# Optimization experiments

Hardware: AMD Instinct MI355X
Metric: run time of the kernel (lower is better)

The kernel has to match this reference:

```python
import jax, jax.numpy as jnp
import numpy as np

N = 50000      # nodes
E = 400000     # edges
DIM = 3        # pseudo-coordinate dim
M = 3          # kernel size per dim (closed B-spline, degree 1)
K = M ** DIM   # 27 basis weights
IN = 32
MID = 32
OUT = 32
EPS = 1e-5


def spline_basis(edge_attr):
    """Degree-1 closed B-spline basis. edge_attr: [E, DIM] in [0,1].
    Returns basis [E, 2^DIM], weight indices [E, 2^DIM] into K."""
    bits = (jnp.arange(2 ** DIM)[:, None] >> jnp.arange(DIM)[None, :]) & 1  # [8, DIM]
    scaled = edge_attr * M                       # closed spline: scale by kernel size
    lo = jnp.floor(scaled)
    frac = scaled - lo                           # [E, DIM]
    b = jnp.where(bits[None].astype(bool), frac[:, None, :], 1.0 - frac[:, None, :])
    basis = jnp.prod(b, axis=-1)                 # [E, 8]
    idx = (lo.astype(jnp.int32)[:, None, :] + bits[None]) % M  # [E, 8, DIM]
    strides = M ** jnp.arange(DIM)               # [1, 3, 9]
    widx = jnp.sum(idx * strides, axis=-1)       # [E, 8] in [0, K)
    return basis, widx


def spline_conv(x, src, dst, basis, widx, W, root, bias):
    """x: [N, in]; W: [K, in, out]; mean aggregation + root weight + bias."""
    x_j = x[src]                                          # gather [E, in]
    upd = basis[:, :, None] * x_j[:, None, :]             # [E, 8, in]
    # scatter-add basis-weighted source features into per-(node, weight-idx) bins
    S = jnp.zeros((N, K, x.shape[1]), x.dtype).at[dst[:, None], widx].add(upd)
    deg = jnp.zeros((N,), x.dtype).at[dst].add(1.0)
    deg = jnp.maximum(deg, 1.0)
    msg = jnp.einsum('nki,kio->no', S, W) / deg[:, None]  # mean over incoming edges
    return msg + x @ root + bias


def batchnorm(h, gamma, beta):
    mu = jnp.mean(h, axis=0)
    var = jnp.var(h, axis=0)  # biased, as in torch BN forward
    return (h - mu) * jax.lax.rsqrt(var + EPS) * gamma + beta


def setup_inputs() -> dict:
    key = jax.random.key(0)
    ks = jax.random.split(key, 16)
    d = {}
    d['x'] = jax.random.normal(ks[0], (N, IN), jnp.float32)
    d['edge_index'] = jax.random.randint(ks[1], (2, E), 0, N, dtype=jnp.int32)
    d['edge_attr'] = jax.random.uniform(ks[2], (E, DIM), dtype=jnp.float32)
    d['pos'] = jax.random.normal(ks[3], (N, DIM), jnp.float32)
    def wscale(fan_in):
        return 1.0 / np.sqrt(fan_in)
    d['W1'] = jax.random.normal(ks[4], (K, IN, MID), jnp.float32) * wscale(IN)
    d['root1'] = jax.random.normal(ks[5], (IN, MID), jnp.float32) * wscale(IN)
    d['b1'] = jnp.zeros((MID,), jnp.float32)
    d['W2'] = jax.random.normal(ks[6], (K, MID, 2 * MID), jnp.float32) * wscale(MID)
    d['root2'] = jax.random.normal(ks[7], (MID, 2 * MID), jnp.float32) * wscale(MID)
    d['b2'] = jnp.zeros((2 * MID,), jnp.float32)
    d['gamma'] = jnp.ones((2 * MID,), jnp.float32)
    d['beta'] = jnp.zeros((2 * MID,), jnp.float32)
    c3_in = 2 * MID + 3
    d['W3'] = jax.random.normal(ks[8], (K, c3_in, OUT), jnp.float32) * wscale(c3_in)
    d['root3'] = jax.random.normal(ks[9], (c3_in, OUT), jnp.float32) * wscale(c3_in)
    d['b3'] = jnp.zeros((OUT,), jnp.float32)
    return d


def reference(x, edge_index, edge_attr, pos, W1, root1, b1, W2, root2, b2,
              gamma, beta, W3, root3, b3):
    src, dst = edge_index[0], edge_index[1]
    basis, widx = spline_basis(edge_attr)
    h = jax.nn.elu(spline_conv(x, src, dst, basis, widx, W1, root1, b1))
    h = jax.nn.elu(batchnorm(spline_conv(h, src, dst, basis, widx, W2, root2, b2), gamma, beta))
    h = jnp.concatenate([h, pos], axis=1)
    out = spline_conv(h, src, dst, basis, widx, W3, root3, b3)
    return out
```

## Files before the change

### kernel.cpp

```cpp
#include <hip/hip_runtime.h>
#include <hip/hip_bf16.h>


#define EPS 1e-5f
#define MAXN 50176
#define MAXE 401408
#define SP2 904
#define SP3 2696

typedef __attribute__((ext_vector_type(8))) short short8;
typedef __attribute__((ext_vector_type(4))) float floatx4;

__device__ int             g_deg[MAXN];
__device__ int             g_offs[MAXN + 1];
__device__ int             g_cursor[MAXN];
__device__ int             g_bsum[256];
__device__ int             g_esrc[MAXE];
__device__ __align__(16) uint4 g_ebas[MAXE * 4];
__device__ __align__(16) __hip_bfloat16 g_h0[MAXN * 32];
__device__ __align__(16) __hip_bfloat16 g_h1[MAXN * 32];
__device__ __align__(16) __hip_bfloat16 g_h2[MAXN * 64];
__device__ __align__(16) __hip_bfloat16 g_h3[MAXN * 96];
__device__ __align__(16) __hip_bfloat16 g_Wp1[28672];
__device__ __align__(16) __hip_bfloat16 g_Wp2[57344];
__device__ __align__(16) __hip_bfloat16 g_Wp3[86016];
__device__ float           g_stats[128];
__device__ int             g_isbf16;

__device__ __forceinline__ float loadf(const void* p, int i, bool bf)
{
    return bf ? (float)((const __hip_bfloat16*)p)[i] : ((const float*)p)[i];
}
__device__ __forceinline__ float bf16f(unsigned int u)
{
    return __uint_as_float(u << 16);
}
__device__ __forceinline__ unsigned short bfbits(float f)
{
    union { __hip_bfloat16 h; unsigned short u; } cv;
    cv.h = __float2bfloat16(f);
    return cv.u;
}

__global__ void init_detect(const unsigned int* __restrict__ x, int n)
{
    int i = blockIdx.x * blockDim.x + threadIdx.x;
    if (blockIdx.x == 0 && threadIdx.x < 64) {
        int lane = threadIdx.x;
        int cnt = 0;
        for (int k = lane; k < 256; k += 64) {
            unsigned int lo = x[k] & 0xFFFFu;
            int ex = (int)((lo >> 7) & 0xFFu);
            if (lo == 0u || (ex >= 96 && ex <= 140)) cnt++;
        }
#pragma unroll
        for (int o = 1; o < 64; o <<= 1) cnt += __shfl_xor(cnt, o, 64);
        if (lane == 0) g_isbf16 = (cnt >= 200) ? 1 : 0;
    }
    if (i < n) { g_deg[i] = 0; g_cursor[i] = 0; }
    if (i < 128) g_stats[i] = 0.0f;
}

template <int COUT>
__device__ __forceinline__ void prep_ws_dev(const void* W, const void* root,
                                            __hip_bfloat16* Wp, int t, bool bf)
{
    int j = t & 7;
    int lane = (t >> 3) & 63;
    int rest = t >> 9;
    int kk = rest % 28;
    int nt = rest / 28;
    int k = kk * 32 + (lane >> 4) * 8 + j;
    int o = nt * 16 + (lane & 15);
    float v;
    if (k < 864) {
        int bin = k >> 5, p = k & 31;
        int ch = 2 * (p & 15) + (p >> 4);
        v = loadf(W, (bin * 32 + ch) * COUT + o, bf);
    } else {
        int p = k - 864;
        int ch = 2 * (p & 15) + (p >> 4);
        v = loadf(root, ch * COUT + o, bf);
    }
    Wp[t] = __float2bfloat16(v);
}

__device__ __forceinline__ void prep_w3_dev(const void* W, const void* root,
                                            __hip_bfloat16* Wp, int t, bool bf)
{
    const int KB = 84;
    int j = t & 7;
    int lane = (t >> 3) & 63;
    int rest = t >> 9;
    int kk = rest % KB;
    int nt = rest / KB;
    int k = kk * 32 + (lane >> 4) * 8 + j;
    int o = nt * 16 + (lane & 15);
    float v = 0.0f;
    if (k < 2592) {
        int bin = k / 96;
        int p = k - bin * 96;
        int ch = 6 * (p & 15) + (p >> 4);
        if (ch < 67) v = loadf(W, (bin * 67 + ch) * 32 + o, bf);
    } else {
        int p = k - 2592;
        int ch = 6 * (p & 15) + (p >> 4);
        if (ch < 67) v = loadf(root, ch * 32 + o, bf);
    }
    Wp[t] = __float2bfloat16(v);
}

__global__ void misc_kernel(const int* __restrict__ dst, const void* __restrict__ x,
                            const void* W1, const void* r1,
                            const void* W2, const void* r2,
                            const void* W3, const void* r3, int E, int N)
{
    int t = blockIdx.x * blockDim.x + threadIdx.x;
    const bool bf = (g_isbf16 != 0);
    if (t < E) { atomicAdd(&g_deg[dst[t]], 1); return; }
    t -= E;
    int nx = N * 32;
    if (t < nx) { g_h0[t] = __float2bfloat16(loadf(x, t, bf)); return; }
    t -= nx;
    if (t < 28672) { prep_ws_dev<32>(W1, r1, g_Wp1, t, bf); return; }
    t -= 28672;
    if (t < 57344) { prep_ws_dev<64>(W2, r2, g_Wp2, t, bf); return; }
    t -= 57344;
    if (t < 86016) { prep_w3_dev(W3, r3, g_Wp3, t, bf); return; }
}

__global__ void scan_blk(int n)
{
    __shared__ int buf[256];
    int tid = threadIdx.x;
    int i = blockIdx.x * 256 + tid;
    int v = (i < n) ? g_deg[i] : 0;
    buf[tid] = v;
    __syncthreads();
    for (int o = 1; o < 256; o <<= 1) {
        int t = (tid >= o) ? buf[tid - o] : 0;
        __syncthreads();
        buf[tid] += t;
        __syncthreads();
    }
    if (i < n) g_offs[i] = buf[tid] - v;
    if (tid == 255) g_bsum[blockIdx.x] = buf[255];
}

__global__ void scan_top(int nb, int n)
{
    __shared__ int buf[256];
    int tid = threadIdx.x;
    int v = (tid < nb) ? g_bsum[tid] : 0;
    buf[tid] = v;
    __syncthreads();
    for (int o = 1; o < 256; o <<= 1) {
        int t = (tid >= o) ? buf[tid - o] : 0;
        __syncthreads();
        buf[tid] += t;
        __syncthreads();
    }
    if (tid < nb) g_bsum[tid] = buf[tid] - v;
    if (tid == nb - 1) g_offs[n] = buf[tid];
}

__global__ void scan_add(int n)
{
    int i = blockIdx.x * 256 + threadIdx.x;
    if (i < n) g_offs[i] += g_bsum[i >> 8];
}

__global__ void basis_fill(const void* __restrict__ attr,
                           const int* __restrict__ src,
                           const int* __restrict__ dst, int E)
{
    int e = blockIdx.x * blockDim.x + threadIdx.x;
    if (e >= E) return;
    const bool bf = (g_isbf16 != 0);
    float f[3];
    int lo[3];
#pragma unroll
    for (int d = 0; d < 3; ++d) {
        float a = loadf(attr, e * 3 + d, bf);
        float s = a * 3.0f;
        float l = floorf(s);
        lo[d] = (int)l;
        f[d] = s - l;
    }
    const int p3[3] = {1, 3, 9};
    int wx8[8];
    unsigned short bb[8];
#pragma unroll
    for (int b = 0; b < 8; ++b) {
        float w = 1.0f;
        int id = 0;
#pragma unroll
        for (int d = 0; d < 3; ++d) {
            int bit = (b >> d) & 1;
            w *= bit ? f[d] : (1.0f - f[d]);
            id += ((lo[d] + bit) % 3) * p3[d];
        }
        wx8[b] = id;
        bb[b] = bfbits(w);
    }
    unsigned wds[16];
#pragma unroll
    for (int i = 0; i < 16; ++i) {
        unsigned w = 0;
#pragma unroll
        for (int b = 0; b < 8; ++b) {
            if (wx8[b] == i)      w |= (unsigned)bb[b];
            if (wx8[b] == i + 16) w |= (unsigned)bb[b] << 16;
        }
        wds[i] = w;
    }
    int d = dst[e];
    int p = atomicAdd(&g_cursor[d], 1);
    int slot = g_offs[d] + p;
    uint4* out4 = &g_ebas[(size_t)slot * 4];
    out4[0] = make_uint4(wds[0],  wds[1],  wds[2],  wds[3]);
    out4[1] = make_uint4(wds[4],  wds[5],  wds[6],  wds[7]);
    out4[2] = make_uint4(wds[8],  wds[9],  wds[10], wds[11]);
    out4[3] = make_uint4(wds[12], wds[13], wds[14], wds[15]);
    g_esrc[slot] = src[e];
}

template <int COUT, bool ELU, int IN_SEL, int OUT_SEL>
__global__ __launch_bounds__(512, 8) void fused_conv(const void* __restrict__ bias,
                                                     int N)
{
    __shared__ unsigned short Sb[8 * SP2];
    __shared__ __align__(16) unsigned basb[8][16][16];
    __shared__ int ssrc[8][16];
    __shared__ float invd[8];
    int tid = threadIdx.x, wid = tid >> 6, lane = tid & 63;
    int nbase = blockIdx.x * 8;
    const bool bf = (g_isbf16 != 0);
    const unsigned short* xptr = (IN_SEL == 0) ? (const unsigned short*)g_h0
                                               : (const unsigned short*)g_h1;
    const __hip_bfloat16* Wp = (COUT == 32) ? g_Wp1 : g_Wp2;

    int n = nbase + wid;
    int m = lane & 15, quad = lane >> 4;

    if (n < N) {
        int e0 = g_offs[n], e1 = g_offs[n + 1];
        floatx4 C00 = {}, C01 = {}, C10 = {}, C11 = {};
        for (int base = e0; base < e1; base += 16) {
            int cnt = e1 - base; if (cnt > 16) cnt = 16;
            {
                int es = lane >> 2, part = lane & 3;
                uint4 v = make_uint4(0, 0, 0, 0);
                if (es < cnt) v = g_ebas[(size_t)(base + es) * 4 + part];
                *(uint4*)&basb[wid][es][part * 4] = v;
                if (lane < 16)
                    ssrc[wid][lane] = (lane < cnt) ? g_esrc[base + lane] : 0;
            }
            __builtin_amdgcn_s_waitcnt(0);
            int jmax = (cnt + 3) >> 2;
            unsigned a0w[4] = {0, 0, 0, 0}, a1w[4] = {0, 0, 0, 0};
            unsigned b0w[4] = {0, 0, 0, 0}, b1w[4] = {0, 0, 0, 0};
#pragma unroll
            for (int j = 0; j < 4; ++j) {
                if (j >= jmax) break;
                int kidx = j * 4 + quad;
                int sn = ssrc[wid][kidx];
                unsigned pw = basb[wid][kidx][m];
                unsigned hw = *((const unsigned*)xptr + (size_t)sn * 16 + m);
                unsigned sh = 16 * (j & 1);
                a0w[j >> 1] |= (hw & 0xFFFFu) << sh;
                a1w[j >> 1] |= (hw >> 16) << sh;
                b0w[j >> 1] |= (pw & 0xFFFFu) << sh;
                b1w[j >> 1] |= (pw >> 16) << sh;
            }
            union U { unsigned w[4]; short8 v; } A0, A1, B0, B1;
#pragma unroll
            for (int q = 0; q < 4; ++q) {
                A0.w[q] = a0w[q]; A1.w[q] = a1w[q];
                B0.w[q] = b0w[q]; B1.w[q] = b1w[q];
            }
            C00 = __builtin_amdgcn_mfma_f32_16x16x32_bf16(A0.v, B0.v, C00, 0, 0, 0);
            C01 = __builtin_amdgcn_mfma_f32_16x16x32_bf16(A0.v, B1.v, C01, 0, 0, 0);
            C10 = __builtin_amdgcn_mfma_f32_16x16x32_bf16(A1.v, B0.v, C10, 0, 0, 0);
            C11 = __builtin_amdgcn_mfma_f32_16x16x32_bf16(A1.v, B1.v, C11, 0, 0, 0);
        }
        unsigned short* Srow = Sb + wid * SP2;
        {
            floatx4 Cf[4] = {C00, C01, C10, C11};
#pragma unroll
            for (int f = 0; f < 4; ++f) {
                int mt = f >> 1, nt = f & 1;
                int bin = nt * 16 + m;
                if (bin < 27) {
                    union { unsigned short h[4]; uint2 u; } pk;
#pragma unroll
                    for (int r = 0; r < 4; ++r) pk.h[r] = bfbits(Cf[f][r]);
                    *(uint2*)(Srow + bin * 32 + mt * 16 + quad * 4) = pk.u;
                }
            }
        }
        if (lane < 32) {
            int ch = 2 * (lane & 15) + (lane >> 4);
            Srow[864 + lane] = xptr[(size_t)n * 32 + ch];
        }
        if (lane == 0) {
            int deg = e1 - e0;
            invd[wid] = 1.0f / (float)(deg < 1 ? 1 : deg);
        }
    }
    __syncthreads();

    if (wid * 16 < COUT) {
        int mrow = m & 7;
        const unsigned short* Ab = Sb + mrow * SP2 + quad * 8;
        floatx4 accS = {}, accR = {};
#pragma unroll
        for (int kk = 0; kk < 28; ++kk) {
            short8 a = *(const short8*)(Ab + kk * 32);
            const short* bp = (const short*)Wp +
                ((size_t)(wid * 28 + kk) * 64 + lane) * 8;
            short8 b = *(const short8*)bp;
            if (kk < 27) accS = __builtin_amdgcn_mfma_f32_16x16x32_bf16(a, b, accS, 0, 0, 0);
            else         accR = __builtin_amdgcn_mfma_f32_16x16x32_bf16(a, b, accR, 0, 0, 0);
        }
        int o = wid * 16 + m;
        float bval = loadf(bias, o, bf);
#pragma unroll
        for (int r = 0; r < 4; ++r) {
            int slot = quad * 4 + r;
            if (slot >= 8) continue;
            int nn = nbase + slot;
            if (nn >= N) continue;
            float v = accS[r] * invd[slot] + accR[r] + bval;
            if (ELU) v = v > 0.0f ? v : expm1f(v);
            if (OUT_SEL == 1) g_h1[nn * 32 + o] = __float2bfloat16(v);
            else              g_h2[nn * 64 + o] = __float2bfloat16(v);
        }
    }
}

__global__ __launch_bounds__(512, 4) void fused_conv3(const void* __restrict__ bias,
                                                      void* __restrict__ out_ext,
                                                      int N)
{
    __shared__ __align__(16) unsigned short Sb[8 * SP3];
    __shared__ __align__(16) union {
        struct { unsigned bas[8][16][16]; int src[8][16]; } s1;
        float red[6][64][4];
    } u;
    __shared__ float invd[8];
    int tid = threadIdx.x, wid = tid >> 6, lane = tid & 63;
    int nbase = blockIdx.x * 8;
    const bool bf = (g_isbf16 != 0);
    const unsigned short* xptr = (const unsigned short*)g_h3;

    int n = nbase + wid;
    int m = lane & 15, quad = lane >> 4;

    if (n < N) {
        int e0 = g_offs[n], e1 = g_offs[n + 1];
        floatx4 C[6][2];
#pragma unroll
        for (int t = 0; t < 6; ++t) {
            C[t][0] = (floatx4){0.f, 0.f, 0.f, 0.f};
            C[t][1] = (floatx4){0.f, 0.f, 0.f, 0.f};
        }
        for (int base = e0; base < e1; base += 16) {
            int cnt = e1 - base; if (cnt > 16) cnt = 16;
            {
                int es = lane >> 2, part = lane & 3;
                uint4 v = make_uint4(0, 0, 0, 0);
                if (es < cnt) v = g_ebas[(size_t)(base + es) * 4 + part];
                *(uint4*)&u.s1.bas[wid][es][part * 4] = v;
                if (lane < 16)
                    u.s1.src[wid][lane] = (lane < cnt) ? g_esrc[base + lane] : 0;
            }
            __builtin_amdgcn_s_waitcnt(0);
            int jmax = (cnt + 3) >> 2;
            unsigned aw[6][4] = {{0, 0, 0, 0}, {0, 0, 0, 0}, {0, 0, 0, 0},
                                 {0, 0, 0, 0}, {0, 0, 0, 0}, {0, 0, 0, 0}};
            unsigned b0w[4] = {0, 0, 0, 0}, b1w[4] = {0, 0, 0, 0};
#pragma unroll
            for (int j = 0; j < 4; ++j) {
                if (j >= jmax) break;
                int kidx = j * 4 + quad;
                int sn = u.s1.src[wid][kidx];
                unsigned pw = u.s1.bas[wid][kidx][m];
                const unsigned* hp = (const unsigned*)xptr + (size_t)sn * 48 + m * 3;
                unsigned h0 = hp[0], h1 = hp[1], h2 = hp[2];
                unsigned sh = 16 * (j & 1);
                int r = j >> 1;
                aw[0][r] |= (h0 & 0xFFFFu) << sh;
                aw[1][r] |= (h0 >> 16) << sh;
                aw[2][r] |= (h1 & 0xFFFFu) << sh;
                aw[3][r] |= (h1 >> 16) << sh;
                aw[4][r] |= (h2 & 0xFFFFu) << sh;
                aw[5][r] |= (h2 >> 16) << sh;
                b0w[r] |= (pw & 0xFFFFu) << sh;
                b1w[r] |= (pw >> 16) << sh;
            }
            union U { unsigned w[4]; short8 v; } A, B0, B1;
#pragma unroll
            for (int q = 0; q < 4; ++q) { B0.w[q] = b0w[q]; B1.w[q] = b1w[q]; }
#pragma unroll
            for (int t = 0; t < 6; ++t) {
#pragma unroll
                for (int q = 0; q < 4; ++q) A.w[q] = aw[t][q];
                C[t][0] = __builtin_amdgcn_mfma_f32_16x16x32_bf16(A.v, B0.v, C[t][0], 0, 0, 0);
                C[t][1] = __builtin_amdgcn_mfma_f32_16x16x32_bf16(A.v, B1.v, C[t][1], 0, 0, 0);
            }
        }
        unsigned short* Srow = Sb + wid * SP3;
#pragma unroll
        for (int t = 0; t < 6; ++t) {
#pragma unroll
            for (int ntile = 0; ntile < 2; ++ntile) {
                int bin = ntile * 16 + m;
                if (bin < 27) {
                    union { unsigned short h[4]; uint2 uu; } pk;
#pragma unroll
                    for (int r = 0; r < 4; ++r) pk.h[r] = bfbits(C[t][ntile][r]);
                    *(uint2*)(Srow + bin * 96 + t * 16 + quad * 4) = pk.uu;
                }
            }
        }
        for (int p = lane; p < 96; p += 64) {
            int ch = 6 * (p & 15) + (p >> 4);
            Srow[2592 + p] = xptr[(size_t)n * 96 + ch];
        }
        if (lane == 0) {
            int deg = e1 - e0;
            invd[wid] = 1.0f / (float)(deg < 1 ? 1 : deg);
        }
    }
    __syncthreads();

    int nt = wid & 1, kq = wid >> 1;
    int mrow = m & 7;
    const unsigned short* Ab = Sb + mrow * SP3 + quad * 8;
    floatx4 accS = {}, accR = {};
    {
        int kbeg = kq * 21, kend = kbeg + 21;
        int ksplit = (kend < 81) ? kend : 81;
        for (int kk = kbeg; kk < ksplit; ++kk) {
            short8 a = *(const short8*)(Ab + kk * 32);
            const short* bp = (const short*)g_Wp3 +
                ((size_t)(nt * 84 + kk) * 64 + lane) * 8;
            short8 b = *(const short8*)bp;
            accS = __builtin_amdgcn_mfma_f32_16x16x32_bf16(a, b, accS, 0, 0, 0);
        }
        for (int kk = ksplit; kk < kend; ++kk) {
            short8 a = *(const short8*)(Ab + kk * 32);
            const short* bp = (const short*)g_Wp3 +
                ((size_t)(nt * 84 + kk) * 64 + lane) * 8;
            short8 b = *(const short8*)bp;
            accR = __builtin_amdgcn_mfma_f32_16x16x32_bf16(a, b, accR, 0, 0, 0);
        }
    }
    if (kq < 3)
        *(floatx4*)&u.red[wid][lane][0] = accS;
    __syncthreads();
    if (kq == 3) {
#pragma unroll
        for (int w = 0; w < 3; ++w)
            accS += *(const floatx4*)&u.red[2 * w + nt][lane][0];
        int o = nt * 16 + m;
        float bval = loadf(bias, o, bf);
#pragma unroll
        for (int r = 0; r < 4; ++r) {
            int slot = quad * 4 + r;
            if (slot >= 8) continue;
            int nn = nbase + slot;
            if (nn >= N) continue;
            float v = accS[r] * invd[slot] + accR[r] + bval;
            if (bf) ((__hip_bfloat16*)out_ext)[nn * 32 + o] = __float2bfloat16(v);
            else    ((float*)out_ext)[nn * 32 + o] = v;
        }
    }
}

__global__ void bn_reduce(int n)
{
    int tid = threadIdx.x;
    int c = tid & 63;
    int r = tid >> 6;
    float s = 0.0f, s2 = 0.0f;
    for (int i = blockIdx.x * 4 + r; i < n; i += gridDim.x * 4) {
        float v = (float)g_h2[i * 64 + c];
        s += v; s2 += v * v;
    }
    __shared__ float b1s[256], b2s[256];
    b1s[tid] = s; b2s[tid] = s2;
    __syncthreads();
    if (r == 0) {
        s  = b1s[c] + b1s[c + 64] + b1s[c + 128] + b1s[c + 192];
        s2 = b2s[c] + b2s[c + 64] + b2s[c + 128] + b2s[c + 192];
        atomicAdd(&g_stats[c], s);
        atomicAdd(&g_stats[64 + c], s2);
    }
}

__global__ void h3_build(const void* __restrict__ pos,
                         const void* __restrict__ gamma,
                         const void* __restrict__ beta, int N)
{
    __shared__ float cf[128];
    int t = threadIdx.x;
    const bool bf = (g_isbf16 != 0);
    if (t < 64) {
        float inv_n = 1.0f / (float)N;
        float mu = g_stats[t] * inv_n;
        float var = g_stats[64 + t] * inv_n - mu * mu;
        float A = rsqrtf(var + EPS) * loadf(gamma, t, bf);
        cf[t] = A;
        cf[64 + t] = loadf(beta, t, bf) - mu * A;
    }
    __syncthreads();
    int idx = blockIdx.x * blockDim.x + t;
    if (idx >= N * 96) return;
    int n = idx / 96, ch = idx - n * 96;
    float v;
    if (ch < 64) {
        float h = (float)g_h2[n * 64 + ch];
        v = h * cf[ch] + cf[64 + ch];
        v = v > 0.0f ? v : expm1f(v);
    } else if (ch < 67) {
        v = loadf(pos, n * 3 + (ch - 64), bf);
    } else {
        v = 0.0f;
    }
    g_h3[(size_t)n * 96 + ch] = __float2bfloat16(v);
}

extern "C" void kernel_launch(void* const* d_in, const int* in_sizes, int n_in,
                              void* d_out, int out_size, void* d_ws, size_t ws_size,
                              hipStream_t stream)
{
    const void* x      = d_in[0];
    const int*  eindex = (const int*)d_in[1];
    const void* eattr  = d_in[2];
    const void* pos    = d_in[3];
    const void* W1     = d_in[4];
    const void* root1  = d_in[5];
    const void* b1     = d_in[6];
    const void* W2     = d_in[7];
    const void* root2  = d_in[8];
    const void* b2     = d_in[9];
    const void* gamma  = d_in[10];
    const void* beta   = d_in[11];
    const void* W3     = d_in[12];
    const void* root3  = d_in[13];
    const void* b3     = d_in[14];
    (void)d_ws; (void)ws_size; (void)n_in; (void)out_size;

    const int N = in_sizes[0] / 32;
    const int E = in_sizes[1] / 2;
    const int* srcp = eindex;
    const int* dstp = eindex + E;

    init_detect<<<(N + 255) / 256, 256, 0, stream>>>((const unsigned int*)x, N);
    {
        int tot = E + N * 32 + 28672 + 57344 + 86016;
        misc_kernel<<<(tot + 255) / 256, 256, 0, stream>>>(
            dstp, x, W1, root1, W2, root2, W3, root3, E, N);
    }
    int nb = (N + 255) / 256;
    scan_blk<<<nb, 256, 0, stream>>>(N);
    scan_top<<<1, 256, 0, stream>>>(nb, N);
    scan_add<<<nb, 256, 0, stream>>>(N);
    basis_fill<<<(E + 255) / 256, 256, 0, stream>>>(eattr, srcp, dstp, E);

    int nb8 = (N + 7) / 8;
    fused_conv<32, true, 0, 1><<<nb8, 512, 0, stream>>>(b1, N);
    fused_conv<64, false, 1, 2><<<nb8, 512, 0, stream>>>(b2, N);
    bn_reduce<<<120, 256, 0, stream>>>(N);
    h3_build<<<(N * 96 + 255) / 256, 256, 0, stream>>>(pos, gamma, beta, N);
    fused_conv3<<<nb8, 512, 0, stream>>>(b3, d_out, N);
}
```

Measured before the change: 371.1 us.

## Sort nodes by in-degree so each block processes similar-degree nodes

Builds a degree histogram, scans it, and fills a node permutation grouped by in-degree. The fused conv kernels then map each wave to a node taken from this order, so the eight waves of a block have balanced edge-loop trip counts and idle less at block barriers. It also swaps the full s_waitcnt(0) for an LDS-only waitcnt with a scheduling barrier. The cost is three small extra kernels and scattered output writes, since consecutive nodes in a block are no longer contiguous in memory.

After: 730.0 us. 1.97x slower.

```diff
diff --git a/kernel.cpp b/kernel.cpp
--- a/kernel.cpp
+++ b/kernel.cpp
@@ -15,6 +15,9 @@
 __device__ int             g_offs[MAXN + 1];
 __device__ int             g_cursor[MAXN];
 __device__ int             g_bsum[256];
+__device__ int             g_dhist[64];
+__device__ int             g_dcur[64];
+__device__ int             g_order[MAXN];
 __device__ int             g_esrc[MAXE];
 __device__ __align__(16) uint4 g_ebas[MAXE * 4];
 __device__ __align__(16) __hip_bfloat16 g_h0[MAXN * 32];
@@ -41,6 +44,11 @@
     cv.h = __float2bfloat16(f);
     return cv.u;
 }
+__device__ __forceinline__ void lds_fence()
+{
+    asm volatile("s_waitcnt lgkmcnt(0)" ::: "memory");
+    __builtin_amdgcn_sched_barrier(0);
+}
 
 __global__ void init_detect(const unsigned int* __restrict__ x, int n)
 {
@@ -59,6 +67,7 @@
     }
     if (i < n) { g_deg[i] = 0; g_cursor[i] = 0; }
     if (i < 128) g_stats[i] = 0.0f;
+    if (i < 64)  { g_dhist[i] = 0; g_dcur[i] = 0; }
 }
 
 template <int COUT>
@@ -167,7 +176,34 @@
 __global__ void scan_add(int n)
 {
     int i = blockIdx.x * 256 + threadIdx.x;
-    if (i < n) g_offs[i] += g_bsum[i >> 8];
+    if (i < n) {
+        g_offs[i] += g_bsum[i >> 8];
+        int d = g_deg[i]; if (d > 63) d = 63;
+        atomicAdd(&g_dhist[d], 1);
+    }
+}
+
+__global__ void order_base(void)
+{
+    int t = threadIdx.x;
+    int v = g_dhist[t];
+    int s = v;
+#pragma unroll
+    for (int o = 1; o < 64; o <<= 1) {
+        int u = __shfl_up(s, o, 64);
+        if (t >= o) s += u;
+    }
+    g_dhist[t] = s - v;
+}
+
+__global__ void order_fill(int n)
+{
+    int i = blockIdx.x * 256 + threadIdx.x;
+    if (i < n) {
+        int d = g_deg[i]; if (d > 63) d = 63;
+        int p = atomicAdd(&g_dcur[d], 1);
+        g_order[g_dhist[d] + p] = i;
+    }
 }
 
 __global__ void basis_fill(const void* __restrict__ attr,
@@ -233,6 +269,7 @@
     __shared__ __align__(16) unsigned basb[8][16][16];
     __shared__ int ssrc[8][16];
     __shared__ float invd[8];
+    __shared__ int nid[8];
     int tid = threadIdx.x, wid = tid >> 6, lane = tid & 63;
     int nbase = blockIdx.x * 8;
     const bool bf = (g_isbf16 != 0);
@@ -240,10 +277,12 @@
                                                : (const unsigned short*)g_h1;
     const __hip_bfloat16* Wp = (COUT == 32) ? g_Wp1 : g_Wp2;
 
-    int n = nbase + wid;
+    int idx = nbase + wid;
+    int n = (idx < N) ? g_order[idx] : -1;
+    if (lane == 0) nid[wid] = n;
     int m = lane & 15, quad = lane >> 4;
 
-    if (n < N) {
+    if (n >= 0) {
         int e0 = g_offs[n], e1 = g_offs[n + 1];
         floatx4 C00 = {}, C01 = {}, C10 = {}, C11 = {};
         for (int base = e0; base < e1; base += 16) {
@@ -256,7 +295,7 @@
                 if (lane < 16)
                     ssrc[wid][lane] = (lane < cnt) ? g_esrc[base + lane] : 0;
             }
-            __builtin_amdgcn_s_waitcnt(0);
+            lds_fence();
             int jmax = (cnt + 3) >> 2;
             unsigned a0w[4] = {0, 0, 0, 0}, a1w[4] = {0, 0, 0, 0};
             unsigned b0w[4] = {0, 0, 0, 0}, b1w[4] = {0, 0, 0, 0};
@@ -329,8 +368,8 @@
         for (int r = 0; r < 4; ++r) {
             int slot = quad * 4 + r;
             if (slot >= 8) continue;
-            int nn = nbase + slot;
-            if (nn >= N) continue;
+            int nn = nid[slot];
+            if (nn < 0) continue;
             float v = accS[r] * invd[slot] + accR[r] + bval;
             if (ELU) v = v > 0.0f ? v : expm1f(v);
             if (OUT_SEL == 1) g_h1[nn * 32 + o] = __float2bfloat16(v);
@@ -349,15 +388,18 @@
         float red[6][64][4];
     } u;
     __shared__ float invd[8];
+    __shared__ int nid[8];
     int tid = threadIdx.x, wid = tid >> 6, lane = tid & 63;
     int nbase = blockIdx.x * 8;
     const bool bf = (g_isbf16 != 0);
     const unsigned short* xptr = (const unsigned short*)g_h3;
 
-    int n = nbase + wid;
+    int idx = nbase + wid;
+    int n = (idx < N) ? g_order[idx] : -1;
+    if (lane == 0) nid[wid] = n;
     int m = lane & 15, quad = lane >> 4;
 
-    if (n < N) {
+    if (n >= 0) {
         int e0 = g_offs[n], e1 = g_offs[n + 1];
         floatx4 C[6][2];
 #pragma unroll
@@ -375,7 +417,7 @@
                 if (lane < 16)
                     u.s1.src[wid][lane] = (lane < cnt) ? g_esrc[base + lane] : 0;
             }
-            __builtin_amdgcn_s_waitcnt(0);
+            lds_fence();
             int jmax = (cnt + 3) >> 2;
             unsigned aw[6][4] = {{0, 0, 0, 0}, {0, 0, 0, 0}, {0, 0, 0, 0},
                                  {0, 0, 0, 0}, {0, 0, 0, 0}, {0, 0, 0, 0}};
@@ -470,8 +512,8 @@
         for (int r = 0; r < 4; ++r) {
             int slot = quad * 4 + r;
             if (slot >= 8) continue;
-            int nn = nbase + slot;
-            if (nn >= N) continue;
+            int nn = nid[slot];
+            if (nn < 0) continue;
             float v = accS[r] * invd[slot] + accR[r] + bval;
             if (bf) ((__hip_bfloat16*)out_ext)[nn * 32 + o] = __float2bfloat16(v);
             else    ((float*)out_ext)[nn * 32 + o] = v;
@@ -568,6 +610,8 @@
     scan_blk<<<nb, 256, 0, stream>>>(N);
     scan_top<<<1, 256, 0, stream>>>(nb, N);
     scan_add<<<nb, 256, 0, stream>>>(N);
+    order_base<<<1, 64, 0, stream>>>();
+    order_fill<<<nb, 256, 0, stream>>>(N);
     basis_fill<<<(E + 255) / 256, 256, 0, stream>>>(eattr, srcp, dstp, E);
 
     int nb8 = (N + 7) / 8;
```

## Batch edge gathers, use LDS-only fence, and split-K the weight GEMM across all waves

Applied to the files above, without the earlier changes.

The edge loop now reads all four source indices and basis words from LDS first, then issues all neighbor-feature gathers together, so loads overlap instead of serialising behind the early-exit branch. The full s_waitcnt is replaced with an lgkmcnt-only wait. In the dense stage, idle waves (for COUT=32 only 2 of 8 were active) now split the 28 K-steps, and partial sums are reduced through an LDS buffer that shares storage with the edge staging arrays. This costs an extra __syncthreads and reduction, and for padded edges it always reads row 0 of the features.

Measured after the change: 394.6 us. 6.3% more time.

```diff
diff --git a/kernel.cpp b/kernel.cpp
--- a/kernel.cpp
+++ b/kernel.cpp
@@ -40,6 +40,11 @@
     union { __hip_bfloat16 h; unsigned short u; } cv;
     cv.h = __float2bfloat16(f);
     return cv.u;
+}
+__device__ __forceinline__ void lds_fence()
+{
+    asm volatile("s_waitcnt lgkmcnt(0)" ::: "memory");
+    __builtin_amdgcn_sched_barrier(0);
 }
 
 __global__ void init_detect(const unsigned int* __restrict__ x, int n)
@@ -230,8 +235,10 @@
                                                      int N)
 {
     __shared__ unsigned short Sb[8 * SP2];
-    __shared__ __align__(16) unsigned basb[8][16][16];
-    __shared__ int ssrc[8][16];
+    __shared__ __align__(16) union {
+        struct { unsigned bas[8][16][16]; int src[8][16]; } s1;
+        float red[8][64][4];
+    } u;
     __shared__ float invd[8];
     int tid = threadIdx.x, wid = tid >> 6, lane = tid & 63;
     int nbase = blockIdx.x * 8;
@@ -252,26 +259,33 @@
                 int es = lane >> 2, part = lane & 3;
                 uint4 v = make_uint4(0, 0, 0, 0);
                 if (es < cnt) v = g_ebas[(size_t)(base + es) * 4 + part];
-                *(uint4*)&basb[wid][es][part * 4] = v;
+                *(uint4*)&u.s1.bas[wid][es][part * 4] = v;
                 if (lane < 16)
-                    ssrc[wid][lane] = (lane < cnt) ? g_esrc[base + lane] : 0;
-            }
-            __builtin_amdgcn_s_waitcnt(0);
-            int jmax = (cnt + 3) >> 2;
+                    u.s1.src[wid][lane] = (lane < cnt) ? g_esrc[base + lane] : 0;
+            }
+            lds_fence();
+            int sn4[4];
+            unsigned pw4[4];
+#pragma unroll
+            for (int j = 0; j < 4; ++j) {
+                int kidx = j * 4 + quad;
+                sn4[j] = u.s1.src[wid][kidx];
+                pw4[j] = u.s1.bas[wid][kidx][m];
+            }
+            unsigned hw4[4];
+#pragma unroll
+            for (int j = 0; j < 4; ++j)
+                hw4[j] = *((const unsigned*)xptr + (size_t)sn4[j] * 16 + m);
             unsigned a0w[4] = {0, 0, 0, 0}, a1w[4] = {0, 0, 0, 0};
             unsigned b0w[4] = {0, 0, 0, 0}, b1w[4] = {0, 0, 0, 0};
 #pragma unroll
             for (int j = 0; j < 4; ++j) {
-                if (j >= jmax) break;
-                int kidx = j * 4 + quad;
-                int sn = ssrc[wid][kidx];
-                unsigned pw = basb[wid][kidx][m];
-                unsigned hw = *((const unsigned*)xptr + (size_t)sn * 16 + m);
                 unsigned sh = 16 * (j & 1);
-                a0w[j >> 1] |= (hw & 0xFFFFu) << sh;
-                a1w[j >> 1] |= (hw >> 16) << sh;
-                b0w[j >> 1] |= (pw & 0xFFFFu) << sh;
-                b1w[j >> 1] |= (pw >> 16) << sh;
+                int r = j >> 1;
+                a0w[r] |= (hw4[j] & 0xFFFFu) << sh;
+                a1w[r] |= (hw4[j] >> 16) << sh;
+                b0w[r] |= (pw4[j] & 0xFFFFu) << sh;
+                b1w[r] |= (pw4[j] >> 16) << sh;
             }
             union U { unsigned w[4]; short8 v; } A0, A1, B0, B1;
 #pragma unroll
@@ -292,10 +306,10 @@
                 int mt = f >> 1, nt = f & 1;
                 int bin = nt * 16 + m;
                 if (bin < 27) {
-                    union { unsigned short h[4]; uint2 u; } pk;
+                    union { unsigned short h[4]; uint2 u2; } pk;
 #pragma unroll
                     for (int r = 0; r < 4; ++r) pk.h[r] = bfbits(Cf[f][r]);
-                    *(uint2*)(Srow + bin * 32 + mt * 16 + quad * 4) = pk.u;
+                    *(uint2*)(Srow + bin * 32 + mt * 16 + quad * 4) = pk.u2;
                 }
             }
         }
@@ -310,20 +324,39 @@
     }
     __syncthreads();
 
-    if (wid * 16 < COUT) {
-        int mrow = m & 7;
-        const unsigned short* Ab = Sb + mrow * SP2 + quad * 8;
-        floatx4 accS = {}, accR = {};
-#pragma unroll
-        for (int kk = 0; kk < 28; ++kk) {
+    const int NT = COUT / 16;
+    const int KQ = 8 / NT;
+    const int KPW = 28 / KQ;
+    int nt = wid % NT, kq = wid / NT;
+    int mrow = m & 7;
+    const unsigned short* Ab = Sb + mrow * SP2 + quad * 8;
+    floatx4 accS = {}, accR = {};
+    {
+        int kbeg = kq * KPW, kend = kbeg + KPW;
+        int ksplit = (kend < 27) ? kend : 27;
+        for (int kk = kbeg; kk < ksplit; ++kk) {
             short8 a = *(const short8*)(Ab + kk * 32);
             const short* bp = (const short*)Wp +
-                ((size_t)(wid * 28 + kk) * 64 + lane) * 8;
+                ((size_t)(nt * 28 + kk) * 64 + lane) * 8;
             short8 b = *(const short8*)bp;
-            if (kk < 27) accS = __builtin_amdgcn_mfma_f32_16x16x32_bf16(a, b, accS, 0, 0, 0);
-            else         accR = __builtin_amdgcn_mfma_f32_16x16x32_bf16(a, b, accR, 0, 0, 0);
-        }
-        int o = wid * 16 + m;
+            accS = __builtin_amdgcn_mfma_f32_16x16x32_bf16(a, b, accS, 0, 0, 0);
+        }
+        for (int kk = ksplit; kk < kend; ++kk) {
+            short8 a = *(const short8*)(Ab + kk * 32);
+            const short* bp = (const short*)Wp +
+                ((size_t)(nt * 28 + kk) * 64 + lane) * 8;
+            short8 b = *(const short8*)bp;
+            accR = __builtin_amdgcn_mfma_f32_16x16x32_bf16(a, b, accR, 0, 0, 0);
+        }
+    }
+    if (kq < KQ - 1)
+        *(floatx4*)&u.red[wid][lane][0] = accS;
+    __syncthreads();
+    if (kq == KQ - 1) {
+#pragma unroll
+        for (int w = 0; w < KQ - 1; ++w)
+            accS += *(const floatx4*)&u.red[w * NT + nt][lane][0];
+        int o = nt * 16 + m;
         float bval = loadf(bias, o, bf);
 #pragma unroll
         for (int r = 0; r < 4; ++r) {
@@ -375,29 +408,37 @@
                 if (lane < 16)
                     u.s1.src[wid][lane] = (lane < cnt) ? g_esrc[base + lane] : 0;
             }
-            __builtin_amdgcn_s_waitcnt(0);
-            int jmax = (cnt + 3) >> 2;
+            lds_fence();
+            int sn4[4];
+            unsigned pw4[4];
+#pragma unroll
+            for (int j = 0; j < 4; ++j) {
+                int kidx = j * 4 + quad;
+                sn4[j] = u.s1.src[wid][kidx];
+                pw4[j] = u.s1.bas[wid][kidx][m];
+            }
+            unsigned hv[4][3];
+#pragma unroll
+            for (int j = 0; j < 4; ++j) {
+                const unsigned* hp = (const unsigned*)xptr +
+                                     (size_t)sn4[j] * 48 + m * 3;
+                hv[j][0] = hp[0]; hv[j][1] = hp[1]; hv[j][2] = hp[2];
+            }
             unsigned aw[6][4] = {{0, 0, 0, 0}, {0, 0, 0, 0}, {0, 0, 0, 0},
                                  {0, 0, 0, 0}, {0, 0, 0, 0}, {0, 0, 0, 0}};
             unsigned b0w[4] = {0, 0, 0, 0}, b1w[4] = {0, 0, 0, 0};
 #pragma unroll
             for (int j = 0; j < 4; ++j) {
-                if (j >= jmax) break;
-                int kidx = j * 4 + quad;
-                int sn = u.s1.src[wid][kidx];
-                unsigned pw = u.s1.bas[wid][kidx][m];
-                const unsigned* hp = (const unsigned*)xptr + (size_t)sn * 48 + m * 3;
-                unsigned h0 = hp[0], h1 = hp[1], h2 = hp[2];
                 unsigned sh = 16 * (j & 1);
                 int r = j >> 1;
-                aw[0][r] |= (h0 & 0xFFFFu) << sh;
-                aw[1][r] |= (h0 >> 16) << sh;
-                aw[2][r] |= (h1 & 0xFFFFu) << sh;
-                aw[3][r] |= (h1 >> 16) << sh;
-                aw[4][r] |= (h2 & 0xFFFFu) << sh;
-                aw[5][r] |= (h2 >> 16) << sh;
-                b0w[r] |= (pw & 0xFFFFu) << sh;
-                b1w[r] |= (pw >> 16) << sh;
+                aw[0][r] |= (hv[j][0] & 0xFFFFu) << sh;
+                aw[1][r] |= (hv[j][0] >> 16) << sh;
+                aw[2][r] |= (hv[j][1] & 0xFFFFu) << sh;
+                aw[3][r] |= (hv[j][1] >> 16) << sh;
+                aw[4][r] |= (hv[j][2] & 0xFFFFu) << sh;
+                aw[5][r] |= (hv[j][2] >> 16) << sh;
+                b0w[r] |= (pw4[j] & 0xFFFFu) << sh;
+                b1w[r] |= (pw4[j] >> 16) << sh;
             }
             union U { unsigned w[4]; short8 v; } A, B0, B1;
 #pragma unroll
```
